# Kernel tuning notes

Measured on AMD Instinct MI355X. Metric: run time of the kernel, lower is better.

## Reference

```python
import jax, jax.numpy as jnp
import numpy as np

ADD_RATE = 0.1


def setup_inputs() -> dict:
    key = jax.random.key(0)
    k1, k2, k3 = jax.random.split(key, 3)
    length, rand_num, D = 4096, 10, 128
    table_len = length + rand_num
    # fixed table built like initiate_by_position: start + i*emb_step + p*pos_step
    start, pos_step, emb_step, sup_val = -0.5, 0.001, 0.0001, -5.0
    pos = start + jnp.arange(length, dtype=jnp.float32) * pos_step          # [length]
    emb = jnp.arange(D, dtype=jnp.float32) * emb_step                        # [D]
    fixed_main = pos[:, None] + emb[None, :]                                  # [length, D]
    fixed_pad = jnp.full((rand_num, D), sup_val, dtype=jnp.float32)
    fixed_table = jnp.concatenate([fixed_main, fixed_pad], axis=0)           # [table_len, D]
    positions = jax.random.randint(k1, (16, 512, 32, 2), 0, table_len, dtype=jnp.int32)
    table_x = jax.random.normal(k2, (table_len, D), dtype=jnp.float32)
    table_y = jax.random.normal(k3, (table_len, D), dtype=jnp.float32)
    return {"positions": positions, "fixed_table": fixed_table,
            "table_x": table_x, "table_y": table_y}


def reference(positions, fixed_table, table_x, table_y):
    # negative indices are remapped to 1 (as in the torch.where)
    idx = jnp.where(positions < 0, 1, positions)                              # [B,M,R,2]
    D = table_x.shape[1]

    def embed(table, idx_slice):
        # scale table by its max, affine-add the fixed table, then gather
        t = ADD_RATE * (table / jnp.max(table)) + fixed_table                 # [table_len, D]
        return t[idx_slice]                                                   # [B,M,R,D]

    ex = embed(table_x, idx[..., 0])
    ey = embed(table_y, idx[..., 1])
    cat = jnp.concatenate([ex, ey], axis=-1)                                  # [B,M,R,2D]
    # view(..., D, 2).sum(-1): sum adjacent pairs of the concatenated vector
    out = cat.reshape(cat.shape[:-1] + (D, 2)).sum(axis=-1)                   # [B,M,R,D]
    return out
```

## Files before the change

### kernel.cpp

```cpp
#include <hip/hip_runtime.h>

typedef float f32x4 __attribute__((ext_vector_type(4)));

#define NBP 128

__global__ __launch_bounds__(256) void table_max_partial(
        const float* __restrict__ tx,
        const float* __restrict__ ty,
        int n4 ,
        float* __restrict__ px,
        float* __restrict__ py) {
    const bool isx = (int)blockIdx.x < NBP;
    const f32x4* t = (const f32x4*)(isx ? tx : ty);
    float* dst = isx ? px : py;
    const int b = isx ? blockIdx.x : blockIdx.x - NBP;
    const int stride = NBP * 256;
    float m = -INFINITY;
    for (int i = b * 256 + threadIdx.x; i < n4; i += stride) {
        const f32x4 v = t[i];
        m = fmaxf(m, fmaxf(fmaxf(v.x, v.y), fmaxf(v.z, v.w)));
    }
    #pragma unroll
    for (int off = 32; off > 0; off >>= 1)
        m = fmaxf(m, __shfl_down(m, off, 64));
    __shared__ float sm[4];
    const int lane = threadIdx.x & 63, wid = threadIdx.x >> 6;
    if (lane == 0) sm[wid] = m;
    __syncthreads();
    if (threadIdx.x == 0)
        dst[b] = fmaxf(fmaxf(sm[0], sm[1]), fmaxf(sm[2], sm[3]));
}

__device__ void reduce_scales(const float* __restrict__ px,
                              const float* __restrict__ py,
                              float& sx, float& sy) {
    float mx = (threadIdx.x < NBP) ? px[threadIdx.x] : -INFINITY;
    float my = (threadIdx.x < NBP) ? py[threadIdx.x] : -INFINITY;
    #pragma unroll
    for (int off = 32; off > 0; off >>= 1) {
        mx = fmaxf(mx, __shfl_down(mx, off, 64));
        my = fmaxf(my, __shfl_down(my, off, 64));
    }
    __shared__ float smx[4], smy[4];
    const int lane = threadIdx.x & 63, wid = threadIdx.x >> 6;
    if (lane == 0) { smx[wid] = mx; smy[wid] = my; }
    __syncthreads();
    sx = 0.1f / fmaxf(fmaxf(smx[0], smx[1]), fmaxf(smx[2], smx[3]));
    sy = 0.1f / fmaxf(fmaxf(smy[0], smy[1]), fmaxf(smy[2], smy[3]));
}

__global__ __launch_bounds__(256) void build_kernel(
        const float* __restrict__ fixedt,
        const float* __restrict__ tx,
        const float* __restrict__ ty,
        const float* __restrict__ px,
        const float* __restrict__ py,
        f32x4* __restrict__ cx, f32x4* __restrict__ cy,
        int total16 ) {
    float sx, sy;
    reduce_scales(px, py, sx, sy);
    const f32x4* fx4 = (const f32x4*)fixedt;
    const f32x4* tx4 = (const f32x4*)tx;
    const f32x4* ty4 = (const f32x4*)ty;
    const int stride = gridDim.x * blockDim.x;
    for (int i = blockIdx.x * blockDim.x + threadIdx.x; i < total16; i += stride) {
        const f32x4 f0 = fx4[2 * i], f1 = fx4[2 * i + 1];
        const f32x4 x0 = tx4[2 * i], x1 = tx4[2 * i + 1];
        const f32x4 y0 = ty4[2 * i], y1 = ty4[2 * i + 1];
        f32x4 cxv, cyv;
        cxv.x = sx * (x0.x + x0.y) + (f0.x + f0.y);
        cxv.y = sx * (x0.z + x0.w) + (f0.z + f0.w);
        cxv.z = sx * (x1.x + x1.y) + (f1.x + f1.y);
        cxv.w = sx * (x1.z + x1.w) + (f1.z + f1.w);
        cyv.x = sy * (y0.x + y0.y) + (f0.x + f0.y);
        cyv.y = sy * (y0.z + y0.w) + (f0.z + f0.w);
        cyv.z = sy * (y1.x + y1.y) + (f1.x + f1.y);
        cyv.w = sy * (y1.z + y1.w) + (f1.z + f1.w);
        cx[i] = cxv;
        cy[i] = cyv;
    }
}

__global__ __launch_bounds__(256) void gather_kernel(
        const int* __restrict__ pos,
        const f32x4* __restrict__ cx,
        const f32x4* __restrict__ cy,
        f32x4* __restrict__ out, int total4) {
    const int stride = gridDim.x * blockDim.x;
    const int i0 = blockIdx.x * blockDim.x + threadIdx.x;
    const int  q    = i0 & 31;
    const bool isx  = (q < 16);
    const f32x4* __restrict__ tab = isx ? cx : cy;
    const int  j    = isx ? q : q - 16;
    const int  poff = isx ? 0 : 1;
    const int  rowstep = stride >> 5;
    int row = i0 >> 5;
    for (int i = i0; i < total4; i += stride, row += rowstep) {
        int p = pos[2 * row + poff];
        if (p < 0) p = 1;
        out[i] = tab[p * 16 + j];
    }
}

extern "C" void kernel_launch(void* const* d_in, const int* in_sizes, int n_in,
                              void* d_out, int out_size, void* d_ws, size_t ws_size,
                              hipStream_t stream) {
    const int*   pos    = (const int*)  d_in[0];
    const float* fixedt = (const float*)d_in[1];
    const float* tx     = (const float*)d_in[2];
    const float* ty     = (const float*)d_in[3];
    f32x4* out = (f32x4*)d_out;

    const int n_table  = in_sizes[2];
    const int rows     = n_table >> 7;
    const int total4   = out_size >> 2;

    float* px = (float*)d_ws;
    float* py = px + NBP;
    f32x4* cx = (f32x4*)(py + NBP);
    f32x4* cy = cx + (size_t)rows * 16;

    table_max_partial<<<2 * NBP, 256, 0, stream>>>(tx, ty, n_table >> 2, px, py);

    const int btot16 = rows * 16;
    build_kernel<<<(btot16 + 255) / 256, 256, 0, stream>>>(fixedt, tx, ty, px, py,
                                                           cx, cy, btot16);
    gather_kernel<<<2048, 256, 0, stream>>>(pos, (const f32x4*)cx, (const f32x4*)cy,
                                            out, total4);
}
```

Baseline: 41.72 us.

## Fuse table build into gather, computing pair-sums on the fly

Drops the separate build kernel that precomputed half-width combined tables. The gather kernel now reads raw table and fixed-table rows at each gathered position and computes the scaled pair-sums inline. This saves one kernel launch and the intermediate table writes. In exchange each output element reads four times as many bytes, since it loads 32 bytes from the raw table and 32 from the fixed table instead of 16 from the precomputed table, and it redoes arithmetic for repeated indices.

```diff
diff --git a/kernel.cpp b/kernel.cpp
--- a/kernel.cpp
+++ b/kernel.cpp
@@ -49,56 +49,44 @@
     sy = 0.1f / fmaxf(fmaxf(smy[0], smy[1]), fmaxf(smy[2], smy[3]));
 }
 
-__global__ __launch_bounds__(256) void build_kernel(
+__global__ __launch_bounds__(256) void gather_direct(
+        const int* __restrict__ pos,
         const float* __restrict__ fixedt,
         const float* __restrict__ tx,
         const float* __restrict__ ty,
         const float* __restrict__ px,
         const float* __restrict__ py,
-        f32x4* __restrict__ cx, f32x4* __restrict__ cy,
-        int total16 ) {
+        f32x4* __restrict__ out, int total4) {
     float sx, sy;
     reduce_scales(px, py, sx, sy);
-    const f32x4* fx4 = (const f32x4*)fixedt;
-    const f32x4* tx4 = (const f32x4*)tx;
-    const f32x4* ty4 = (const f32x4*)ty;
-    const int stride = gridDim.x * blockDim.x;
-    for (int i = blockIdx.x * blockDim.x + threadIdx.x; i < total16; i += stride) {
-        const f32x4 f0 = fx4[2 * i], f1 = fx4[2 * i + 1];
-        const f32x4 x0 = tx4[2 * i], x1 = tx4[2 * i + 1];
-        const f32x4 y0 = ty4[2 * i], y1 = ty4[2 * i + 1];
-        f32x4 cxv, cyv;
-        cxv.x = sx * (x0.x + x0.y) + (f0.x + f0.y);
-        cxv.y = sx * (x0.z + x0.w) + (f0.z + f0.w);
-        cxv.z = sx * (x1.x + x1.y) + (f1.x + f1.y);
-        cxv.w = sx * (x1.z + x1.w) + (f1.z + f1.w);
-        cyv.x = sy * (y0.x + y0.y) + (f0.x + f0.y);
-        cyv.y = sy * (y0.z + y0.w) + (f0.z + f0.w);
-        cyv.z = sy * (y1.x + y1.y) + (f1.x + f1.y);
-        cyv.w = sy * (y1.z + y1.w) + (f1.z + f1.w);
-        cx[i] = cxv;
-        cy[i] = cyv;
-    }
-}
 
-__global__ __launch_bounds__(256) void gather_kernel(
-        const int* __restrict__ pos,
-        const f32x4* __restrict__ cx,
-        const f32x4* __restrict__ cy,
-        f32x4* __restrict__ out, int total4) {
     const int stride = gridDim.x * blockDim.x;
     const int i0 = blockIdx.x * blockDim.x + threadIdx.x;
     const int  q    = i0 & 31;
     const bool isx  = (q < 16);
-    const f32x4* __restrict__ tab = isx ? cx : cy;
-    const int  j    = isx ? q : q - 16;
+    const float s   = isx ? sx : sy;
+    const int  j2   = (isx ? q : q - 16) * 2;
+    const f32x4* __restrict__ tab = (const f32x4*)(isx ? tx : ty) + j2;
+    const f32x4* __restrict__ fx4 = (const f32x4*)fixedt + j2;
     const int  poff = isx ? 0 : 1;
     const int  rowstep = stride >> 5;
+
     int row = i0 >> 5;
     for (int i = i0; i < total4; i += stride, row += rowstep) {
         int p = pos[2 * row + poff];
         if (p < 0) p = 1;
-        out[i] = tab[p * 16 + j];
+        const f32x4* tsrc = tab + p * 32;
+        const f32x4* fsrc = fx4 + p * 32;
+        const f32x4 t0 = tsrc[0];
+        const f32x4 t1 = tsrc[1];
+        const f32x4 f0 = fsrc[0];
+        const f32x4 f1 = fsrc[1];
+        f32x4 v;
+        v.x = s * (t0.x + t0.y) + (f0.x + f0.y);
+        v.y = s * (t0.z + t0.w) + (f0.z + f0.w);
+        v.z = s * (t1.x + t1.y) + (f1.x + f1.y);
+        v.w = s * (t1.z + t1.w) + (f1.z + f1.w);
+        out[i] = v;
     }
 }
 
@@ -112,19 +100,12 @@
     f32x4* out = (f32x4*)d_out;
 
     const int n_table  = in_sizes[2];
-    const int rows     = n_table >> 7;
     const int total4   = out_size >> 2;
 
     float* px = (float*)d_ws;
     float* py = px + NBP;
-    f32x4* cx = (f32x4*)(py + NBP);
-    f32x4* cy = cx + (size_t)rows * 16;
 
     table_max_partial<<<2 * NBP, 256, 0, stream>>>(tx, ty, n_table >> 2, px, py);
-
-    const int btot16 = rows * 16;
-    build_kernel<<<(btot16 + 255) / 256, 256, 0, stream>>>(fixedt, tx, ty, px, py,
-                                                           cx, cy, btot16);
-    gather_kernel<<<2048, 256, 0, stream>>>(pos, (const f32x4*)cx, (const f32x4*)cy,
+    gather_direct<<<2048, 256, 0, stream>>>(pos, fixedt, tx, ty, px, py,
                                             out, total4);
 }
```

After: 69.90 us. 67.6% more time.
